# Kernel optimization log

Measured on AMD Instinct MI355X. Metric: run time of the kernel, lower is better.

Reference implementation:

```python
import jax, jax.numpy as jnp
import numpy as np

TEMPERATURE = 1.0
TOP_K = 50
TOP_P = 0.95
NEG_INF = float('-inf')


def setup_inputs() -> dict:
    key = jax.random.key(0)
    k1, k2, k3, k4 = jax.random.split(key, 4)
    B, S, D, V = 32, 8, 1024, 50257
    psi_real = jax.random.normal(k1, (B, S, D), dtype=jnp.float32)
    psi_imag = jax.random.normal(k2, (B, S, D), dtype=jnp.float32)
    W_real = jax.random.normal(k3, (V, D), dtype=jnp.float32) * 0.02
    W_imag = jax.random.normal(k4, (V, D), dtype=jnp.float32) * 0.02
    bias = jnp.zeros((V,), dtype=jnp.float32)
    return {"psi_real": psi_real, "psi_imag": psi_imag, "W_real": W_real,
            "W_imag": W_imag, "bias": bias}


def _legacy_filter(logits, temperature, top_k, top_p):
    # temperature
    l = logits / max(temperature, 1e-8)
    # top-k: keep values >= k-th largest
    if 0 < top_k < l.shape[-1]:
        topk_vals = jax.lax.top_k(l, top_k)[0]          # [B,S,k]
        threshold = topk_vals[..., -1:]
        l = jnp.where(l < threshold, NEG_INF, l)
    # top-p (nucleus): mask tokens where exclusive cumulative prob >= p
    if top_p < 1.0:
        p = max(top_p, 1e-6)
        order = jnp.argsort(-l, axis=-1)                # descending
        sl = jnp.take_along_axis(l, order, axis=-1)
        sp = jax.nn.softmax(sl, axis=-1)
        cum = jnp.cumsum(sp, axis=-1)
        mask = (cum - sp) >= p                          # exclusive cumsum >= p
        mask = mask.at[..., 0].set(False)               # always keep top token
        sl = jnp.where(mask, NEG_INF, sl)
        inv = jnp.argsort(order, axis=-1)               # scatter back to original order
        l = jnp.take_along_axis(sl, inv, axis=-1)
    return l


def reference(psi_real, psi_imag, W_real, W_imag, bias):
    # logits = proj_real(psi.real) + proj_imag(psi.imag) + bias  -> [B,S,V]
    logits = (jnp.einsum('bsd,vd->bsv', psi_real, W_real)
              + jnp.einsum('bsd,vd->bsv', psi_imag, W_imag) + bias)
    sampling_logits = _legacy_filter(logits, TEMPERATURE, TOP_K, TOP_P)
    probs = jax.nn.softmax(sampling_logits, axis=-1)
    # multinomial(probs, 1) == categorical over filtered logits
    tokens = jax.random.categorical(jax.random.key(42), sampling_logits, axis=-1)
    log_probs = jax.nn.log_softmax(logits, axis=-1)
    return logits, tokens, probs, log_probs
```

## Files before the change

### kernel.cpp

```cpp
#include <hip/hip_runtime.h>
#include <stdint.h>
#include <math.h>

#define MM 256
#define KD 1024
#define K2 2048
#define VV 50257
#define NF4 (VV / 4)
#define NSTEP 32

static constexpr size_t OUT_TOKENS = (size_t)MM * VV;
static constexpr size_t OUT_PROBS  = OUT_TOKENS + MM;
static constexpr size_t OUT_LOGPR  = OUT_PROBS + (size_t)MM * VV;

#define WS_ABUF_BYTES (1u * 1024u * 1024u)

typedef __attribute__((ext_vector_type(8))) _Float16 f16x8;
typedef __attribute__((ext_vector_type(4))) float f32x4;

__device__ __forceinline__ unsigned rotl32(unsigned x, int r) {
  return (x << r) | (x >> (32 - r));
}

__device__ __forceinline__ uint2 threefry2x32(unsigned k0, unsigned k1,
                                              unsigned x0, unsigned x1) {
  unsigned ks[3] = {k0, k1, k0 ^ k1 ^ 0x1BD11BDAu};
  const int rot[8] = {13, 15, 26, 6, 17, 29, 16, 24};
  x0 += ks[0]; x1 += ks[1];
  #pragma unroll
  for (int g = 0; g < 5; ++g) {
    const int base = (g & 1) ? 4 : 0;
    #pragma unroll
    for (int i = 0; i < 4; ++i) {
      x0 += x1;
      x1 = rotl32(x1, rot[base + i]);
      x1 ^= x0;
    }
    x0 += ks[(g + 1) % 3];
    x1 += ks[(g + 2) % 3] + (unsigned)(g + 1);
  }
  return make_uint2(x0, x1);
}

__device__ __forceinline__ float gumbel_at(unsigned flat) {
  uint2 r = threefry2x32(0u, 42u, 0u, flat);
  unsigned w = r.x ^ r.y;
  unsigned fb = (w >> 9) | 0x3F800000u;
  float f = __uint_as_float(fb) - 1.0f;
  const float tiny = 1.1754943508222875e-38f;
  float u = fmaxf(tiny, f + tiny);
  float t1 = (float)log((double)u);
  float t3 = (float)log((double)(-t1));
  return -t3;
}

__global__ __launch_bounds__(256)
void k_prep(const float* __restrict__ psi_r, const float* __restrict__ psi_i,
            ushort* __restrict__ a_buf) {
  int t = blockIdx.x * 256 + threadIdx.x;
  int lane = t & 63;
  int mb = (t >> 6) & 15;
  int s = t >> 10;
  int lr = lane & 15, lg = lane >> 4;
  int m = mb * 16 + lr;
  int kloc = (s & 31) * 32 + lg * 8;
  const float* __restrict__ src = (s < 32) ? psi_r : psi_i;
  float4 v0 = *reinterpret_cast<const float4*>(&src[m * KD + kloc]);
  float4 v1 = *reinterpret_cast<const float4*>(&src[m * KD + kloc + 4]);
  float in[8] = {v0.x, v0.y, v0.z, v0.w, v1.x, v1.y, v1.z, v1.w};
  _Float16 h[8];
  #pragma unroll
  for (int j = 0; j < 8; ++j) h[j] = (_Float16)in[j];
  size_t base = (size_t)(s * 16 + mb) * 512 + (size_t)lane * 8;
  *reinterpret_cast<uint4*>(&a_buf[base]) = *reinterpret_cast<uint4*>(h);
}

#define BN 64
#define BK 64
#define GT 256

struct W4 { float4 a, b, c, d; };
struct A4 { uint4 h[4]; };

__device__ __forceinline__ void loadW(W4& w, const float* __restrict__ Wr,
                                      const float* __restrict__ Wi,
                                      int t, int gn, int bcol) {
  const float* __restrict__ Bs = (t < 16) ? Wr : Wi;
  int ko = (t << 6) & (KD - 1);
  if (gn < VV) {
    const float* p = &Bs[(size_t)gn * KD + ko + bcol];
    w.a = *reinterpret_cast<const float4*>(p);
    w.b = *reinterpret_cast<const float4*>(p + 4);
    w.c = *reinterpret_cast<const float4*>(p + 8);
    w.d = *reinterpret_cast<const float4*>(p + 12);
  }
}

__device__ __forceinline__ void stageW(const W4& w, ushort* __restrict__ bh,
                                       int eo0, int eo1) {
  float in[16] = {w.a.x, w.a.y, w.a.z, w.a.w, w.b.x, w.b.y, w.b.z, w.b.w,
                  w.c.x, w.c.y, w.c.z, w.c.w, w.d.x, w.d.y, w.d.z, w.d.w};
  _Float16 h[16];
  #pragma unroll
  for (int j = 0; j < 16; ++j) h[j] = (_Float16)in[j];
  *reinterpret_cast<uint4*>(&bh[eo0]) = reinterpret_cast<uint4*>(h)[0];
  *reinterpret_cast<uint4*>(&bh[eo1]) = reinterpret_cast<uint4*>(h)[1];
}

__device__ __forceinline__ void loadA(A4& A, const uint4* __restrict__ a_buf,
                                      int s, int kq, int wid, int lane) {
  #pragma unroll
  for (int mi = 0; mi < 4; ++mi) {
    int chunk = ((s * 2 + kq) * 16) + wid * 4 + mi;
    A.h[mi] = a_buf[(size_t)chunk * 64 + lane];
  }
}

__device__ __forceinline__ void computeKQ(f32x4 (&acc)[4][4], const A4& A,
                                          const ushort* __restrict__ bhp,
                                          int kq, int lr, int lg) {
  f16x8 bh[4];
  #pragma unroll
  for (int ni = 0; ni < 4; ++ni) {
    int r = ni * 16 + lr;
    int eoff = r * BK + ((kq * 32 + lg * 8) ^ ((r & 7) << 3));
    bh[ni] = *reinterpret_cast<const f16x8*>(&bhp[eoff]);
  }
  __builtin_amdgcn_s_setprio(1);
  #pragma unroll
  for (int mi = 0; mi < 4; ++mi) {
    f16x8 ah = *reinterpret_cast<const f16x8*>(&A.h[mi]);
    #pragma unroll
    for (int ni = 0; ni < 4; ++ni)
      acc[mi][ni] = __builtin_amdgcn_mfma_f32_16x16x32_f16(ah, bh[ni], acc[mi][ni], 0, 0, 0);
  }
  __builtin_amdgcn_s_setprio(0);
}

__global__ __launch_bounds__(GT, 2)
void k_gemm(const uint4* __restrict__ a_buf,
            const float* __restrict__ Wr, const float* __restrict__ Wi,
            const float* __restrict__ bias, float* __restrict__ logits) {
  __shared__ ushort sB[2][BN * BK];

  const int tid  = threadIdx.x;
  const int lane = tid & 63;
  const int wid  = tid >> 6;
  const int vb   = blockIdx.x * BN;
  const int lr = lane & 15;
  const int lg = lane >> 4;

  const int brow = tid >> 2;
  const int bcol = (tid & 3) << 4;
  const int gn   = vb + brow;
  const int eo0  = brow * BK + (bcol ^ ((brow & 7) << 3));
  const int eo1  = brow * BK + ((bcol + 8) ^ ((brow & 7) << 3));

  f32x4 acc[4][4];
  #pragma unroll
  for (int i = 0; i < 4; ++i)
    #pragma unroll
    for (int j = 0; j < 4; ++j)
      #pragma unroll
      for (int q = 0; q < 4; ++q) acc[i][j][q] = 0.f;

  W4 wX, wY;
  wX.a = wX.b = wX.c = wX.d = make_float4(0.f, 0.f, 0.f, 0.f);
  wY = wX;
  A4 A0, A1;
  loadW(wX, Wr, Wi, 0, gn, bcol);
  loadW(wY, Wr, Wi, 1, gn, bcol);
  loadA(A0, a_buf, 0, 0, wid, lane);
  stageW(wX, &sB[0][0], eo0, eo1);
  loadW(wX, Wr, Wi, 2, gn, bcol);
  asm volatile("s_waitcnt lgkmcnt(0)" ::: "memory");
  asm volatile("s_barrier" ::: "memory");

  for (int sp = 0; sp < NSTEP / 2; ++sp) {
    const int s0 = sp * 2;
    const int s1 = s0 + 1;
    loadA(A1, a_buf, s0, 1, wid, lane);
    stageW(wY, &sB[1][0], eo0, eo1);
    if (s0 + 3 < NSTEP) loadW(wY, Wr, Wi, s0 + 3, gn, bcol);
    computeKQ(acc, A0, &sB[0][0], 0, lr, lg);
    loadA(A0, a_buf, s1, 0, wid, lane);
    computeKQ(acc, A1, &sB[0][0], 1, lr, lg);
    asm volatile("s_waitcnt lgkmcnt(0)" ::: "memory");
    asm volatile("s_barrier" ::: "memory");
    loadA(A1, a_buf, s1, 1, wid, lane);
    if (s1 + 1 < NSTEP) stageW(wX, &sB[0][0], eo0, eo1);
    if (s1 + 3 < NSTEP) loadW(wX, Wr, Wi, s1 + 3, gn, bcol);
    computeKQ(acc, A0, &sB[1][0], 0, lr, lg);
    if (s1 < NSTEP - 1) loadA(A0, a_buf, s1 + 1, 0, wid, lane);
    computeKQ(acc, A1, &sB[1][0], 1, lr, lg);
    asm volatile("s_waitcnt lgkmcnt(0)" ::: "memory");
    asm volatile("s_barrier" ::: "memory");
  }

  #pragma unroll
  for (int ni = 0; ni < 4; ++ni) {
    int n = vb + ni * 16 + lr;
    if (n < VV) {
      float b = bias[n];
      #pragma unroll
      for (int mi = 0; mi < 4; ++mi) {
        #pragma unroll
        for (int j = 0; j < 4; ++j) {
          int m = wid * 64 + mi * 16 + lg * 4 + j;
          logits[(size_t)m * VV + n] = acc[mi][ni][j] + b;
        }
      }
    }
  }
}

__device__ __forceinline__ unsigned ordf(float f) {
  unsigned u = __float_as_uint(f);
  return u ^ ((u >> 31) ? 0xFFFFFFFFu : 0x80000000u);
}

#define HREP 4
#define HSTRIDE 4097

__global__ __launch_bounds__(1024)
void k_stats(const float* __restrict__ logits, float* __restrict__ ws4) {
  const int row = blockIdx.x;
  const int tid = threadIdx.x;
  const float* __restrict__ x = logits + (size_t)row * VV;

  __shared__ unsigned hist[HREP * HSTRIDE];
  __shared__ float pm[16], ps[16];

  for (int i = tid; i < HREP * HSTRIDE; i += 1024) hist[i] = 0u;
  __syncthreads();

  const int rep = (tid & 3) * HSTRIDE;
  float lm = -INFINITY, ls = 0.f;
  for (int i4 = tid; i4 < NF4; i4 += 1024) {
    float4 v4 = *reinterpret_cast<const float4*>(&x[i4 * 4]);
    float vs[4] = {v4.x, v4.y, v4.z, v4.w};
    #pragma unroll
    for (int j = 0; j < 4; ++j) {
      float v = vs[j];
      atomicAdd(&hist[rep + (ordf(v) >> 20)], 1u);
      if (v <= lm) {
        ls += expf(v - lm);
      } else {
        ls = ls * expf(lm - v) + 1.f;
        lm = v;
      }
    }
  }
  if (tid == 0) {
    float v = x[VV - 1];
    atomicAdd(&hist[ordf(v) >> 20], 1u);
    if (v <= lm) ls += expf(v - lm);
    else { ls = ls * expf(lm - v) + 1.f; lm = v; }
  }
  #pragma unroll
  for (int off = 32; off; off >>= 1) {
    float om = __shfl_xor(lm, off);
    float os = __shfl_xor(ls, off);
    float M = fmaxf(lm, om);
    ls = ls * expf(lm - M) + os * expf(om - M);
    lm = M;
  }
  if ((tid & 63) == 0) { pm[tid >> 6] = lm; ps[tid >> 6] = ls; }
  __syncthreads();

  for (int b = tid; b < 4096; b += 1024)
    hist[b] = hist[b] + hist[HSTRIDE + b] + hist[2 * HSTRIDE + b] + hist[3 * HSTRIDE + b];
  __syncthreads();

  if (tid < 64) {
    float m2 = (tid < 16) ? pm[tid] : -3e38f;
    float s2 = (tid < 16) ? ps[tid] : 0.f;
    #pragma unroll
    for (int off = 8; off; off >>= 1) {
      float om = __shfl_xor(m2, off);
      float os = __shfl_xor(s2, off);
      float M = fmaxf(m2, om);
      s2 = s2 * expf(m2 - M) + os * expf(om - M);
      m2 = M;
    }
    unsigned seg = 0;
    #pragma unroll 8
    for (int b = 0; b < 64; ++b) seg += hist[tid * 64 + ((b + tid) & 63)];
    unsigned suf = seg;
    #pragma unroll
    for (int off = 1; off < 64; off <<= 1) {
      unsigned o = __shfl_down(suf, off);
      if (tid + off < 64) suf += o;
    }
    unsigned long long mk = __ballot(suf >= 50u);
    int lstar = 63 - __builtin_clzll(mk);
    unsigned above = (lstar < 63) ? (unsigned)__shfl((int)suf, lstar + 1) : 0u;
    if (tid == 0) {
      unsigned cum = above;
      int bin = lstar * 64;
      for (int b = 63; b >= 0; --b) {
        cum += hist[lstar * 64 + b];
        if (cum >= 50u) { bin = lstar * 64 + b; break; }
      }
      bin = (bin > 0) ? bin - 1 : 0;
      ws4[row * 4 + 0] = m2;
      ws4[row * 4 + 1] = logf(s2);
      ws4[row * 4 + 2] = __uint_as_float((unsigned)bin << 20);
    }
  }
}

#define CAP 1024
#define NSEL 56

__global__ __launch_bounds__(1024)
void k_post(const float* __restrict__ logits, const float* __restrict__ ws4,
            const float* __restrict__ psi_r, const float* __restrict__ psi_i,
            const float* __restrict__ Wr, const float* __restrict__ Wi,
            const float* __restrict__ bias,
            float* __restrict__ logpr, float* __restrict__ probs,
            float* __restrict__ tokens) {
  const int row = blockIdx.x;
  const int tid = threadIdx.x;
  const float* __restrict__ x = logits + (size_t)row * VV;
  float* __restrict__ lp = logpr + (size_t)row * VV;
  float* __restrict__ pr = probs + (size_t)row * VV;

  __shared__ float cv[CAP];
  __shared__ int   ci[CAP];
  __shared__ unsigned s_cnt;
  __shared__ float top_v[NSEL];
  __shared__ int   top_i[NSEL];
  __shared__ float srt_v[50];
  __shared__ int   srt_i[50];
  __shared__ int   s_nsel;

  if (tid == 0) s_cnt = 0u;
  __syncthreads();

  const float mx = ws4[row * 4 + 0];
  const float lz = ws4[row * 4 + 1];
  const unsigned lo = __float_as_uint(ws4[row * 4 + 2]);
  const float4 z4 = make_float4(0.f, 0.f, 0.f, 0.f);

  for (int i4 = tid; i4 < NF4; i4 += 1024) {
    float4 v = *reinterpret_cast<const float4*>(&x[i4 * 4]);
    *reinterpret_cast<float4*>(&lp[i4 * 4]) =
        make_float4((v.x - mx) - lz, (v.y - mx) - lz,
                    (v.z - mx) - lz, (v.w - mx) - lz);
    *reinterpret_cast<float4*>(&pr[i4 * 4]) = z4;
    float vs[4] = {v.x, v.y, v.z, v.w};
    #pragma unroll
    for (int j = 0; j < 4; ++j) {
      if (ordf(vs[j]) >= lo) {
        unsigned pos = atomicAdd(&s_cnt, 1u);
        if (pos < CAP) { cv[pos] = vs[j]; ci[pos] = i4 * 4 + j; }
      }
    }
  }
  if (tid == 0) {
    float v = x[VV - 1];
    lp[VV - 1] = (v - mx) - lz;
    pr[VV - 1] = 0.f;
    if (ordf(v) >= lo) {
      unsigned pos = atomicAdd(&s_cnt, 1u);
      if (pos < CAP) { cv[pos] = v; ci[pos] = VV - 1; }
    }
  }
  __syncthreads();
  const int ncand = (int)min(s_cnt, (unsigned)CAP);

  if (tid < 64) {
    for (int it = 0; it < NSEL; ++it) {
      float bv = -INFINITY;
      int bi = 0x7FFFFFFF, bs = 0;
      for (int c = tid; c < ncand; c += 64) {
        float v = cv[c];
        int id = ci[c];
        if (v > bv || (v == bv && id < bi)) { bv = v; bi = id; bs = c; }
      }
      #pragma unroll
      for (int off = 32; off; off >>= 1) {
        float ov = __shfl_xor(bv, off);
        int oi = __shfl_xor(bi, off);
        int os = __shfl_xor(bs, off);
        if (ov > bv || (ov == bv && oi < bi)) { bv = ov; bi = oi; bs = os; }
      }
      if (tid == 0) {
        top_v[it] = bv;
        top_i[it] = bi;
        cv[bs] = -INFINITY;
      }
    }
    if (tid == 0) s_nsel = (ncand < NSEL) ? ncand : NSEL;
  }
  __syncthreads();
  const int nsel = s_nsel;

  {
    const int wv = tid >> 6, ln = tid & 63;
    const float* __restrict__ prr = psi_r + (size_t)row * KD;
    const float* __restrict__ pii = psi_i + (size_t)row * KD;
    for (int j = wv; j < nsel; j += 16) {
      int idx = top_i[j];
      const float* __restrict__ wr = Wr + (size_t)idx * KD;
      const float* __restrict__ wi = Wi + (size_t)idx * KD;
      double ar = 0.0, ai = 0.0;
      for (int k = ln; k < KD; k += 64) {
        ar += (double)prr[k] * (double)wr[k];
        ai += (double)pii[k] * (double)wi[k];
      }
      #pragma unroll
      for (int off = 32; off; off >>= 1) {
        ar += __shfl_xor(ar, off);
        ai += __shfl_xor(ai, off);
      }
      if (ln == 0) top_v[j] = ((float)ar + (float)ai) + bias[idx];
    }
  }
  __syncthreads();

  if (tid < 64) {
    float v = (tid < nsel) ? top_v[tid] : -INFINITY;
    int id = (tid < nsel) ? top_i[tid] : 0x7FFFFFFF;
    for (int it = 0; it < 50; ++it) {
      float bv = v;
      int bi = id, bl = tid;
      #pragma unroll
      for (int off = 32; off; off >>= 1) {
        float ov = __shfl_xor(bv, off);
        int oi = __shfl_xor(bi, off);
        int ol = __shfl_xor(bl, off);
        if (ov > bv || (ov == bv && oi < bi)) { bv = ov; bi = oi; bl = ol; }
      }
      if (tid == 0) { srt_v[it] = bv; srt_i[it] = bi; }
      if (tid == bl) { v = -INFINITY; id = 0x7FFFFFFF; }
    }

    float tv = (tid < 50) ? srt_v[tid] : -3e38f;
    float m0 = srt_v[0];
    float sp = (tid < 50) ? expf(tv - m0) : 0.f;
    float Z = sp;
    #pragma unroll
    for (int off = 32; off; off >>= 1) Z += __shfl_xor(Z, off);
    float pref = sp;
    #pragma unroll
    for (int off = 1; off < 64; off <<= 1) {
      float o = __shfl_up(pref, off);
      if (tid >= off) pref += o;
    }
    float excl = (pref - sp) / Z;
    bool keep = (tid < 50) && ((tid == 0) || (excl < 0.95f));
    float spk = keep ? sp : 0.f;
    float Z2 = spk;
    #pragma unroll
    for (int off = 32; off; off >>= 1) Z2 += __shfl_xor(Z2, off);

    float bt = -3e38f;
    int bidx = 0x7FFFFFFF;
    if (keep) {
      int idx = srt_i[tid];
      pr[idx] = sp / Z2;
      bt = tv + gumbel_at((unsigned)((size_t)row * VV + idx));
      bidx = idx;
    }
    #pragma unroll
    for (int off = 32; off; off >>= 1) {
      float ot = __shfl_xor(bt, off);
      int oi = __shfl_xor(bidx, off);
      if (ot > bt || (ot == bt && oi < bidx)) { bt = ot; bidx = oi; }
    }
    if (tid == 0) tokens[row] = (float)bidx;
  }
}

extern "C" void kernel_launch(void* const* d_in, const int* in_sizes, int n_in,
                              void* d_out, int out_size, void* d_ws, size_t ws_size,
                              hipStream_t stream) {
  const float* psi_r = (const float*)d_in[0];
  const float* psi_i = (const float*)d_in[1];
  const float* Wr    = (const float*)d_in[2];
  const float* Wi    = (const float*)d_in[3];
  const float* bias  = (const float*)d_in[4];
  float* out = (float*)d_out;

  ushort* a_buf = (ushort*)d_ws;
  float* ws4    = (float*)((char*)d_ws + WS_ABUF_BYTES);

  float* logits = out;
  float* tokens = out + OUT_TOKENS;
  float* probs  = out + OUT_PROBS;
  float* logpr  = out + OUT_LOGPR;

  k_prep<<<256, 256, 0, stream>>>(psi_r, psi_i, a_buf);
  const int nblk = (VV + BN - 1) / BN;
  k_gemm<<<nblk, GT, 0, stream>>>((const uint4*)a_buf, Wr, Wi, bias, logits);
  k_stats<<<MM, 1024, 0, stream>>>(logits, ws4);
  k_post<<<MM, 1024, 0, stream>>>(logits, ws4, psi_r, psi_i, Wr, Wi, bias,
                                  logpr, probs, tokens);
}
```

Measured before the change: 323.8 us.

## Drop LDS staging in GEMM and fuse stats/post kernels into one

```diff
diff --git a/kernel.cpp b/kernel.cpp
--- a/kernel.cpp
+++ b/kernel.cpp
@@ -12,8 +12,6 @@
 static constexpr size_t OUT_TOKENS = (size_t)MM * VV;
 static constexpr size_t OUT_PROBS  = OUT_TOKENS + MM;
 static constexpr size_t OUT_LOGPR  = OUT_PROBS + (size_t)MM * VV;
-
-#define WS_ABUF_BYTES (1u * 1024u * 1024u)
 
 typedef __attribute__((ext_vector_type(8))) _Float16 f16x8;
 typedef __attribute__((ext_vector_type(4))) float f32x4;
@@ -76,73 +74,21 @@
 }
 
 #define BN 64
-#define BK 64
 #define GT 256
 
-struct W4 { float4 a, b, c, d; };
-struct A4 { uint4 h[4]; };
-
-__device__ __forceinline__ void loadW(W4& w, const float* __restrict__ Wr,
-                                      const float* __restrict__ Wi,
-                                      int t, int gn, int bcol) {
-  const float* __restrict__ Bs = (t < 16) ? Wr : Wi;
-  int ko = (t << 6) & (KD - 1);
-  if (gn < VV) {
-    const float* p = &Bs[(size_t)gn * KD + ko + bcol];
-    w.a = *reinterpret_cast<const float4*>(p);
-    w.b = *reinterpret_cast<const float4*>(p + 4);
-    w.c = *reinterpret_cast<const float4*>(p + 8);
-    w.d = *reinterpret_cast<const float4*>(p + 12);
-  }
-}
-
-__device__ __forceinline__ void stageW(const W4& w, ushort* __restrict__ bh,
-                                       int eo0, int eo1) {
-  float in[16] = {w.a.x, w.a.y, w.a.z, w.a.w, w.b.x, w.b.y, w.b.z, w.b.w,
-                  w.c.x, w.c.y, w.c.z, w.c.w, w.d.x, w.d.y, w.d.z, w.d.w};
-  _Float16 h[16];
-  #pragma unroll
-  for (int j = 0; j < 16; ++j) h[j] = (_Float16)in[j];
-  *reinterpret_cast<uint4*>(&bh[eo0]) = reinterpret_cast<uint4*>(h)[0];
-  *reinterpret_cast<uint4*>(&bh[eo1]) = reinterpret_cast<uint4*>(h)[1];
-}
-
-__device__ __forceinline__ void loadA(A4& A, const uint4* __restrict__ a_buf,
-                                      int s, int kq, int wid, int lane) {
-  #pragma unroll
-  for (int mi = 0; mi < 4; ++mi) {
-    int chunk = ((s * 2 + kq) * 16) + wid * 4 + mi;
-    A.h[mi] = a_buf[(size_t)chunk * 64 + lane];
-  }
-}
-
-__device__ __forceinline__ void computeKQ(f32x4 (&acc)[4][4], const A4& A,
-                                          const ushort* __restrict__ bhp,
-                                          int kq, int lr, int lg) {
-  f16x8 bh[4];
-  #pragma unroll
-  for (int ni = 0; ni < 4; ++ni) {
-    int r = ni * 16 + lr;
-    int eoff = r * BK + ((kq * 32 + lg * 8) ^ ((r & 7) << 3));
-    bh[ni] = *reinterpret_cast<const f16x8*>(&bhp[eoff]);
-  }
-  __builtin_amdgcn_s_setprio(1);
-  #pragma unroll
-  for (int mi = 0; mi < 4; ++mi) {
-    f16x8 ah = *reinterpret_cast<const f16x8*>(&A.h[mi]);
-    #pragma unroll
-    for (int ni = 0; ni < 4; ++ni)
-      acc[mi][ni] = __builtin_amdgcn_mfma_f32_16x16x32_f16(ah, bh[ni], acc[mi][ni], 0, 0, 0);
-  }
-  __builtin_amdgcn_s_setprio(0);
-}
-
-__global__ __launch_bounds__(GT, 2)
+__device__ __forceinline__ f16x8 cvt8(float4 x, float4 y) {
+  f16x8 r;
+  r[0] = (_Float16)x.x; r[1] = (_Float16)x.y;
+  r[2] = (_Float16)x.z; r[3] = (_Float16)x.w;
+  r[4] = (_Float16)y.x; r[5] = (_Float16)y.y;
+  r[6] = (_Float16)y.z; r[7] = (_Float16)y.w;
+  return r;
+}
+
+__global__ __launch_bounds__(GT, 3)
 void k_gemm(const uint4* __restrict__ a_buf,
             const float* __restrict__ Wr, const float* __restrict__ Wi,
             const float* __restrict__ bias, float* __restrict__ logits) {
-  __shared__ ushort sB[2][BN * BK];
-
   const int tid  = threadIdx.x;
   const int lane = tid & 63;
   const int wid  = tid >> 6;
@@ -150,11 +96,12 @@
   const int lr = lane & 15;
   const int lg = lane >> 4;
 
-  const int brow = tid >> 2;
-  const int bcol = (tid & 3) << 4;
-  const int gn   = vb + brow;
-  const int eo0  = brow * BK + (bcol ^ ((brow & 7) << 3));
-  const int eo1  = brow * BK + ((bcol + 8) ^ ((brow & 7) << 3));
+  int gnc[4];
+  #pragma unroll
+  for (int ni = 0; ni < 4; ++ni) {
+    int gn = vb + ni * 16 + lr;
+    gnc[ni] = (gn < VV) ? gn : (VV - 1);
+  }
 
   f32x4 acc[4][4];
   #pragma unroll
@@ -164,37 +111,58 @@
       #pragma unroll
       for (int q = 0; q < 4; ++q) acc[i][j][q] = 0.f;
 
-  W4 wX, wY;
-  wX.a = wX.b = wX.c = wX.d = make_float4(0.f, 0.f, 0.f, 0.f);
-  wY = wX;
-  A4 A0, A1;
-  loadW(wX, Wr, Wi, 0, gn, bcol);
-  loadW(wY, Wr, Wi, 1, gn, bcol);
-  loadA(A0, a_buf, 0, 0, wid, lane);
-  stageW(wX, &sB[0][0], eo0, eo1);
-  loadW(wX, Wr, Wi, 2, gn, bcol);
-  asm volatile("s_waitcnt lgkmcnt(0)" ::: "memory");
-  asm volatile("s_barrier" ::: "memory");
-
-  for (int sp = 0; sp < NSTEP / 2; ++sp) {
-    const int s0 = sp * 2;
-    const int s1 = s0 + 1;
-    loadA(A1, a_buf, s0, 1, wid, lane);
-    stageW(wY, &sB[1][0], eo0, eo1);
-    if (s0 + 3 < NSTEP) loadW(wY, Wr, Wi, s0 + 3, gn, bcol);
-    computeKQ(acc, A0, &sB[0][0], 0, lr, lg);
-    loadA(A0, a_buf, s1, 0, wid, lane);
-    computeKQ(acc, A1, &sB[0][0], 1, lr, lg);
-    asm volatile("s_waitcnt lgkmcnt(0)" ::: "memory");
-    asm volatile("s_barrier" ::: "memory");
-    loadA(A1, a_buf, s1, 1, wid, lane);
-    if (s1 + 1 < NSTEP) stageW(wX, &sB[0][0], eo0, eo1);
-    if (s1 + 3 < NSTEP) loadW(wX, Wr, Wi, s1 + 3, gn, bcol);
-    computeKQ(acc, A0, &sB[1][0], 0, lr, lg);
-    if (s1 < NSTEP - 1) loadA(A0, a_buf, s1 + 1, 0, wid, lane);
-    computeKQ(acc, A1, &sB[1][0], 1, lr, lg);
-    asm volatile("s_waitcnt lgkmcnt(0)" ::: "memory");
-    asm volatile("s_barrier" ::: "memory");
+  #pragma unroll 2
+  for (int s = 0; s < NSTEP; ++s) {
+    const float* __restrict__ Bs = (s < 16) ? Wr : Wi;
+    const int ko = (s & 15) * 64 + lg * 8;
+
+    uint4 a0[4];
+    #pragma unroll
+    for (int mi = 0; mi < 4; ++mi)
+      a0[mi] = a_buf[(size_t)((s * 2 + 0) * 16 + wid * 4 + mi) * 64 + lane];
+    float4 b0a[4], b0b[4];
+    #pragma unroll
+    for (int ni = 0; ni < 4; ++ni) {
+      const float* p = Bs + (size_t)gnc[ni] * KD + ko;
+      b0a[ni] = *reinterpret_cast<const float4*>(p);
+      b0b[ni] = *reinterpret_cast<const float4*>(p + 4);
+    }
+    uint4 a1[4];
+    #pragma unroll
+    for (int mi = 0; mi < 4; ++mi)
+      a1[mi] = a_buf[(size_t)((s * 2 + 1) * 16 + wid * 4 + mi) * 64 + lane];
+    float4 b1a[4], b1b[4];
+    #pragma unroll
+    for (int ni = 0; ni < 4; ++ni) {
+      const float* p = Bs + (size_t)gnc[ni] * KD + ko + 32;
+      b1a[ni] = *reinterpret_cast<const float4*>(p);
+      b1b[ni] = *reinterpret_cast<const float4*>(p + 4);
+    }
+
+    f16x8 b16[4];
+    #pragma unroll
+    for (int ni = 0; ni < 4; ++ni) b16[ni] = cvt8(b0a[ni], b0b[ni]);
+    __builtin_amdgcn_s_setprio(1);
+    #pragma unroll
+    for (int mi = 0; mi < 4; ++mi) {
+      f16x8 ah = *reinterpret_cast<const f16x8*>(&a0[mi]);
+      #pragma unroll
+      for (int ni = 0; ni < 4; ++ni)
+        acc[mi][ni] = __builtin_amdgcn_mfma_f32_16x16x32_f16(ah, b16[ni], acc[mi][ni], 0, 0, 0);
+    }
+    __builtin_amdgcn_s_setprio(0);
+
+    #pragma unroll
+    for (int ni = 0; ni < 4; ++ni) b16[ni] = cvt8(b1a[ni], b1b[ni]);
+    __builtin_amdgcn_s_setprio(1);
+    #pragma unroll
+    for (int mi = 0; mi < 4; ++mi) {
+      f16x8 ah = *reinterpret_cast<const f16x8*>(&a1[mi]);
+      #pragma unroll
+      for (int ni = 0; ni < 4; ++ni)
+        acc[mi][ni] = __builtin_amdgcn_mfma_f32_16x16x32_f16(ah, b16[ni], acc[mi][ni], 0, 0, 0);
+    }
+    __builtin_amdgcn_s_setprio(0);
   }
 
   #pragma unroll
@@ -221,17 +189,37 @@
 
 #define HREP 4
 #define HSTRIDE 4097
+#define CAP 1024
+#define NSEL 56
 
 __global__ __launch_bounds__(1024)
-void k_stats(const float* __restrict__ logits, float* __restrict__ ws4) {
+void k_fused(const float* __restrict__ logits,
+             const float* __restrict__ psi_r, const float* __restrict__ psi_i,
+             const float* __restrict__ Wr, const float* __restrict__ Wi,
+             const float* __restrict__ bias,
+             float* __restrict__ logpr, float* __restrict__ probs,
+             float* __restrict__ tokens) {
   const int row = blockIdx.x;
   const int tid = threadIdx.x;
   const float* __restrict__ x = logits + (size_t)row * VV;
+  float* __restrict__ lp = logpr + (size_t)row * VV;
+  float* __restrict__ pr = probs + (size_t)row * VV;
 
   __shared__ unsigned hist[HREP * HSTRIDE];
   __shared__ float pm[16], ps[16];
+  __shared__ float cv[CAP];
+  __shared__ int   ci[CAP];
+  __shared__ unsigned s_cnt;
+  __shared__ float s_mx, s_lz;
+  __shared__ unsigned s_lo;
+  __shared__ float top_v[NSEL];
+  __shared__ int   top_i[NSEL];
+  __shared__ float srt_v[50];
+  __shared__ int   srt_i[50];
+  __shared__ int   s_nsel;
 
   for (int i = tid; i < HREP * HSTRIDE; i += 1024) hist[i] = 0u;
+  if (tid == 0) s_cnt = 0u;
   __syncthreads();
 
   const int rep = (tid & 3) * HSTRIDE;
@@ -303,44 +291,16 @@
         if (cum >= 50u) { bin = lstar * 64 + b; break; }
       }
       bin = (bin > 0) ? bin - 1 : 0;
-      ws4[row * 4 + 0] = m2;
-      ws4[row * 4 + 1] = logf(s2);
-      ws4[row * 4 + 2] = __uint_as_float((unsigned)bin << 20);
-    }
-  }
-}
-
-#define CAP 1024
-#define NSEL 56
-
-__global__ __launch_bounds__(1024)
-void k_post(const float* __restrict__ logits, const float* __restrict__ ws4,
-            const float* __restrict__ psi_r, const float* __restrict__ psi_i,
-            const float* __restrict__ Wr, const float* __restrict__ Wi,
-            const float* __restrict__ bias,
-            float* __restrict__ logpr, float* __restrict__ probs,
-            float* __restrict__ tokens) {
-  const int row = blockIdx.x;
-  const int tid = threadIdx.x;
-  const float* __restrict__ x = logits + (size_t)row * VV;
-  float* __restrict__ lp = logpr + (size_t)row * VV;
-  float* __restrict__ pr = probs + (size_t)row * VV;
-
-  __shared__ float cv[CAP];
-  __shared__ int   ci[CAP];
-  __shared__ unsigned s_cnt;
-  __shared__ float top_v[NSEL];
-  __shared__ int   top_i[NSEL];
-  __shared__ float srt_v[50];
-  __shared__ int   srt_i[50];
-  __shared__ int   s_nsel;
-
-  if (tid == 0) s_cnt = 0u;
-  __syncthreads();
-
-  const float mx = ws4[row * 4 + 0];
-  const float lz = ws4[row * 4 + 1];
-  const unsigned lo = __float_as_uint(ws4[row * 4 + 2]);
+      s_mx = m2;
+      s_lz = logf(s2);
+      s_lo = (unsigned)bin << 20;
+    }
+  }
+  __syncthreads();
+
+  const float mx = s_mx;
+  const float lz = s_lz;
+  const unsigned lo = s_lo;
   const float4 z4 = make_float4(0.f, 0.f, 0.f, 0.f);
 
   for (int i4 = tid; i4 < NF4; i4 += 1024) {
@@ -485,7 +445,6 @@
   float* out = (float*)d_out;
 
   ushort* a_buf = (ushort*)d_ws;
-  float* ws4    = (float*)((char*)d_ws + WS_ABUF_BYTES);
 
   float* logits = out;
   float* tokens = out + OUT_TOKENS;
@@ -495,7 +454,6 @@
   k_prep<<<256, 256, 0, stream>>>(psi_r, psi_i, a_buf);
   const int nblk = (VV + BN - 1) / BN;
   k_gemm<<<nblk, GT, 0, stream>>>((const uint4*)a_buf, Wr, Wi, bias, logits);
-  k_stats<<<MM, 1024, 0, stream>>>(logits, ws4);
-  k_post<<<MM, 1024, 0, stream>>>(logits, ws4, psi_r, psi_i, Wr, Wi, bias,
-                                  logpr, probs, tokens);
-}
+  k_fused<<<MM, 1024, 0, stream>>>(logits, psi_r, psi_i, Wr, Wi, bias,
+                                   logpr, probs, tokens);
+}
```

Measured after the change: 468.6 us. 44.7% more time.
